# Kernel tuning notes

Hardware: AMD Instinct MI355X
Metric: run time of the kernel (lower is better)

## Reference

```python
import jax, jax.numpy as jnp
import numpy as np

E, T, IN, OUT, GS = 8, 2048, 2048, 2048, 64


def setup_inputs() -> dict:
    key = jax.random.key(0)
    k1, k2, k3, k4, k5 = jax.random.split(key, 5)
    x = jax.random.normal(k1, (T, IN), dtype=jnp.float32)
    # int4 codes in [0,16): stored unpacked as int32 for the reference
    qweight = jax.random.randint(k2, (E, IN, OUT), 0, 16, dtype=jnp.int32)
    G = IN // GS  # quant groups along the reduction dim
    scales = jax.random.uniform(k3, (E, G, OUT), jnp.float32, minval=0.005, maxval=0.02)
    zeros = jax.random.normal(k4, (E, G, OUT), jnp.float32) * 0.01
    scales_and_zeros = jnp.stack([scales, zeros], axis=-1)  # [E, G, OUT, 2]
    # tokens sorted by expert: per-expert counts are diffs of sorted cut points, sum == T
    cuts = jnp.sort(jax.random.randint(k5, (E - 1,), 0, T + 1, dtype=jnp.int32))
    bounds = jnp.concatenate([jnp.zeros((1,), jnp.int32), cuts, jnp.full((1,), T, jnp.int32)])
    tokens_per_expert = jnp.diff(bounds).astype(jnp.int32)  # [E]
    return {
        "x": x,
        "qweight": qweight,
        "scales_and_zeros": scales_and_zeros,
        "tokens_per_expert": tokens_per_expert,
        "group_size": GS,
    }


def reference(x, qweight, scales_and_zeros, tokens_per_expert, group_size):
    """Grouped (per-expert) int4 dequant + GEMM over an expert-sorted token matrix.

    Math of aten._weight_int4pack_mm per expert e over each quant group g:
        W_e[k, n] = (q_e[k, n] - 8) * scale_e[g, n] + zero_e[g, n],  g = k // group_size
        out[rows_e] = x[rows_e] @ W_e
    where rows_e is the contiguous slice given by cumsum(tokens_per_expert).
    """
    n_exp, in_f, out_f = qweight.shape
    n_tok = x.shape[0]
    G = in_f // group_size

    # dequantize all expert weights: [E, IN, OUT]
    q = qweight.reshape(n_exp, G, group_size, out_f).astype(x.dtype)
    scales = scales_and_zeros[..., 0][:, :, None, :]  # [E, G, 1, OUT]
    zeros = scales_and_zeros[..., 1][:, :, None, :]   # [E, G, 1, OUT]
    W = ((q - 8.0) * scales + zeros).reshape(n_exp, in_f, out_f)

    # expert id per token from the cumsum boundaries (tokens are expert-sorted)
    cum = jnp.cumsum(tokens_per_expert)                                # [E]
    eid = jnp.searchsorted(cum, jnp.arange(n_tok), side="right")       # [T]
    onehot = (eid[:, None] == jnp.arange(n_exp)[None, :]).astype(x.dtype)  # [T, E]

    # dispatch -> per-expert GEMM -> combine (jit-safe grouped GEMM)
    xe = jnp.einsum("te,ti->eti", onehot, x)       # [E, T, IN]
    ye = jnp.einsum("eti,eio->eto", xe, W)         # [E, T, OUT]
    out = jnp.einsum("te,eto->to", onehot, ye)     # [T, OUT]
    return out
```

## Files before the change

### kernel.cpp

```cpp
#include <hip/hip_runtime.h>
#include <hip/hip_bf16.h>

constexpr int NE  = 8;
constexpr int T   = 2048;
constexpr int IN  = 2048;
constexpr int OUT = 2048;
constexpr int GS  = 64;
constexpr int G   = IN / GS;

constexpr int BM = 128;
constexpr int BN = 64;
constexpr int BK = 64;
constexpr int NTILE = IN / BK;
constexpr int LDB = BK + 8;

using short8  = __attribute__((ext_vector_type(8))) short;
using short4v = __attribute__((ext_vector_type(4))) short;
using floatx4 = __attribute__((ext_vector_type(4))) float;
using int4v   = __attribute__((ext_vector_type(4))) int;
using float4v = __attribute__((ext_vector_type(4))) float;

__global__ __launch_bounds__(256)
void cvt_x_bf16(const float* __restrict__ x, __hip_bfloat16* __restrict__ xb) {
    const int i = (blockIdx.x * 256 + threadIdx.x) * 4;
    const float4 v = *(const float4*)(x + i);
    union { unsigned long long u; __hip_bfloat162 h2[2]; } p;
    p.h2[0] = __float22bfloat162_rn(float2{v.x, v.y});
    p.h2[1] = __float22bfloat162_rn(float2{v.z, v.w});
    *(unsigned long long*)(xb + i) = p.u;
}

__global__ __launch_bounds__(256, 4)
void hqq_grouped_gemm(const __hip_bfloat16* __restrict__ xb,
                      const int*   __restrict__ qw,
                      const float* __restrict__ snz,
                      const int*   __restrict__ tpe,
                      float* __restrict__ out) {
    const int tid = threadIdx.x;
    const int e   = blockIdx.z;
    const int tm  = blockIdx.y;
    const int n0  = blockIdx.x * BN;

    int b0 = 0;
#pragma unroll
    for (int i = 0; i < NE; ++i) { int c = tpe[i]; if (i < e) b0 += c; }
    const int b1 = b0 + tpe[e];
    const int row0 = b0 + tm * BM;
    if (row0 >= b1) return;

    __shared__ __hip_bfloat16 Bs[2][BN][LDB];

    floatx4 acc[2][4];
#pragma unroll
    for (int i = 0; i < 2; ++i)
#pragma unroll
        for (int j = 0; j < 4; ++j)
            acc[i][j] = (floatx4){0.f, 0.f, 0.f, 0.f};

    const int n4 = (tid & 15) * 4;
    const int kq = (tid >> 4) * 4;

    const int lane = tid & 63;
    const int wid  = tid >> 6;
    const int wm = wid * 32;
    const int lm = lane & 15;
    const int lk = (lane >> 4) * 8;

    const int*    qbase  = qw + (size_t)e * IN * OUT + n0 + n4;
    const float2* szbase = (const float2*)snz + (size_t)e * G * OUT + n0 + n4;

    int4v   qvA[4], qvB[4];
    float4v szA[2], szB[2];

    auto issue = [&](int t, int4v (&qv)[4], float4v (&sz)[2]) {
        const int k0 = t * BK;
        const float4v* szp = (const float4v*)(szbase + (size_t)(k0 >> 6) * OUT);
        sz[0] = szp[0];
        sz[1] = szp[1];
#pragma unroll
        for (int kk = 0; kk < 4; ++kk)
            qv[kk] = *(const int4v*)(qbase + (size_t)(k0 + kq + kk) * OUT);
    };

    auto stage = [&](__hip_bfloat16 (&B)[BN][LDB], int4v (&qv)[4], float4v (&sz)[2]) {
#pragma unroll
        for (int nn = 0; nn < 4; ++nn) {
            const float sc = sz[nn >> 1][(nn & 1) * 2];
            const float cc = sz[nn >> 1][(nn & 1) * 2 + 1] - 8.0f * sc;
            union { short4v v; __hip_bfloat162 h2[2]; } pb;
            pb.h2[0] = __float22bfloat162_rn(float2{(float)qv[0][nn] * sc + cc,
                                                    (float)qv[1][nn] * sc + cc});
            pb.h2[1] = __float22bfloat162_rn(float2{(float)qv[2][nn] * sc + cc,
                                                    (float)qv[3][nn] * sc + cc});
            *(short4v*)&B[n4 + nn][kq] = pb.v;
        }
    };

    auto mfma_tile = [&](const __hip_bfloat16 (&B)[BN][LDB], int k0) {
#pragma unroll
        for (int ks = 0; ks < BK; ks += 32) {
            short8 af[2], bfr[4];
#pragma unroll
            for (int i = 0; i < 2; ++i) {
                const int row = row0 + wm + i * 16 + lm;
                const int rr  = row < b1 ? row : (b1 - 1);
                af[i] = *(const short8*)(xb + (size_t)rr * IN + k0 + ks + lk);
            }
#pragma unroll
            for (int j = 0; j < 4; ++j)
                bfr[j] = *(const short8*)&B[j * 16 + lm][ks + lk];
#pragma unroll
            for (int i = 0; i < 2; ++i)
#pragma unroll
                for (int j = 0; j < 4; ++j)
                    acc[i][j] = __builtin_amdgcn_mfma_f32_16x16x32_bf16(
                        af[i], bfr[j], acc[i][j], 0, 0, 0);
        }
    };

#define TILE_SYNC()                                          \
    asm volatile("s_waitcnt lgkmcnt(0)" ::: "memory");       \
    __builtin_amdgcn_s_barrier();                            \
    __builtin_amdgcn_sched_barrier(0)

    issue(0, qvA, szA);

    for (int t = 0; t < NTILE; t += 2) {
        stage(Bs[0], qvA, szA);
        issue(t + 1, qvB, szB);
        TILE_SYNC();
        mfma_tile(Bs[0], t * BK);

        stage(Bs[1], qvB, szB);
        issue(t + 2 < NTILE ? t + 2 : t + 1, qvA, szA);
        TILE_SYNC();
        mfma_tile(Bs[1], (t + 1) * BK);
    }
#undef TILE_SYNC

    const int lq = (lane >> 4) * 4;
#pragma unroll
    for (int i = 0; i < 2; ++i) {
#pragma unroll
        for (int r = 0; r < 4; ++r) {
            const int row = row0 + wm + i * 16 + lq + r;
            if (row < b1) {
                float* op = out + (size_t)row * OUT + n0 + lm;
#pragma unroll
                for (int j = 0; j < 4; ++j)
                    op[j * 16] = acc[i][j][r];
            }
        }
    }
}

extern "C" void kernel_launch(void* const* d_in, const int* in_sizes, int n_in,
                              void* d_out, int out_size, void* d_ws, size_t ws_size,
                              hipStream_t stream) {
    const float* x   = (const float*)d_in[0];
    const int*   qw  = (const int*)d_in[1];
    const float* snz = (const float*)d_in[2];
    const int*   tpe = (const int*)d_in[3];
    float* out = (float*)d_out;
    __hip_bfloat16* xb = (__hip_bfloat16*)d_ws;

    cvt_x_bf16<<<(T * IN) / (256 * 4), 256, 0, stream>>>(x, xb);

    dim3 grid(OUT / BN, T / BM, NE);
    hqq_grouped_gemm<<<grid, 256, 0, stream>>>(xb, qw, snz, tpe, out);
}
```

Before: 265.2 us.

## Prefetch A fragments two tiles ahead and XOR-swizzle unpadded LDS B tile

Activation fragments for the MFMA now load into registers one to two tiles ahead instead of being fetched inside the compute loop. The quantized-weight prefetch is also deepened to two tiles in flight. The padded LDS row stride is replaced by an XOR swizzle on the k offset, which keeps bank-conflict avoidance while shrinking LDS. The extra live registers lead to lowering the launch-bounds occupancy hint from 4 to 3 blocks per CU.

```diff
diff --git a/kernel.cpp b/kernel.cpp
--- a/kernel.cpp
+++ b/kernel.cpp
@@ -12,7 +12,7 @@
 constexpr int BN = 64;
 constexpr int BK = 64;
 constexpr int NTILE = IN / BK;
-constexpr int LDB = BK + 8;
+constexpr int LDB = 64;
 
 using short8  = __attribute__((ext_vector_type(8))) short;
 using short4v = __attribute__((ext_vector_type(4))) short;
@@ -30,7 +30,7 @@
     *(unsigned long long*)(xb + i) = p.u;
 }
 
-__global__ __launch_bounds__(256, 4)
+__global__ __launch_bounds__(256, 3)
 void hqq_grouped_gemm(const __hip_bfloat16* __restrict__ xb,
                       const int*   __restrict__ qw,
                       const float* __restrict__ snz,
@@ -57,29 +57,45 @@
         for (int j = 0; j < 4; ++j)
             acc[i][j] = (floatx4){0.f, 0.f, 0.f, 0.f};
 
-    const int n4 = (tid & 15) * 4;
-    const int kq = (tid >> 4) * 4;
+    const int n4  = (tid & 15) * 4;
+    const int kq4 = (tid >> 4) * 4;
+    const int wsz = (tid & 3) << 4;
 
     const int lane = tid & 63;
     const int wid  = tid >> 6;
     const int wm = wid * 32;
     const int lm = lane & 15;
     const int lk = (lane >> 4) * 8;
+    const int rsz = ((lm >> 2) & 3) << 4;
 
     const int*    qbase  = qw + (size_t)e * IN * OUT + n0 + n4;
     const float2* szbase = (const float2*)snz + (size_t)e * G * OUT + n0 + n4;
 
+    const int r0c = min(row0 + wm + lm,      b1 - 1);
+    const int r1c = min(row0 + wm + 16 + lm, b1 - 1);
+    const __hip_bfloat16* ap0 = xb + (size_t)r0c * IN + lk;
+    const __hip_bfloat16* ap1 = xb + (size_t)r1c * IN + lk;
+
     int4v   qvA[4], qvB[4];
     float4v szA[2], szB[2];
+    short8  afA[4], afB[4];
 
-    auto issue = [&](int t, int4v (&qv)[4], float4v (&sz)[2]) {
+    auto issue_q = [&](int t, int4v (&qv)[4], float4v (&sz)[2]) {
         const int k0 = t * BK;
         const float4v* szp = (const float4v*)(szbase + (size_t)(k0 >> 6) * OUT);
         sz[0] = szp[0];
         sz[1] = szp[1];
 #pragma unroll
         for (int kk = 0; kk < 4; ++kk)
-            qv[kk] = *(const int4v*)(qbase + (size_t)(k0 + kq + kk) * OUT);
+            qv[kk] = *(const int4v*)(qbase + (size_t)(k0 + kq4 + kk) * OUT);
+    };
+
+    auto issue_af = [&](int t, short8 (&af)[4]) {
+        const int k0 = t * BK;
+        af[0] = *(const short8*)(ap0 + k0);
+        af[1] = *(const short8*)(ap1 + k0);
+        af[2] = *(const short8*)(ap0 + k0 + 32);
+        af[3] = *(const short8*)(ap1 + k0 + 32);
     };
 
     auto stage = [&](__hip_bfloat16 (&B)[BN][LDB], int4v (&qv)[4], float4v (&sz)[2]) {
@@ -92,29 +108,23 @@
                                                     (float)qv[1][nn] * sc + cc});
             pb.h2[1] = __float22bfloat162_rn(float2{(float)qv[2][nn] * sc + cc,
                                                     (float)qv[3][nn] * sc + cc});
-            *(short4v*)&B[n4 + nn][kq] = pb.v;
+            *(short4v*)&B[n4 + nn][kq4 ^ wsz] = pb.v;
         }
     };
 
-    auto mfma_tile = [&](const __hip_bfloat16 (&B)[BN][LDB], int k0) {
+    auto mfma_tile = [&](const __hip_bfloat16 (&B)[BN][LDB], const short8 (&af)[4]) {
 #pragma unroll
-        for (int ks = 0; ks < BK; ks += 32) {
-            short8 af[2], bfr[4];
-#pragma unroll
-            for (int i = 0; i < 2; ++i) {
-                const int row = row0 + wm + i * 16 + lm;
-                const int rr  = row < b1 ? row : (b1 - 1);
-                af[i] = *(const short8*)(xb + (size_t)rr * IN + k0 + ks + lk);
-            }
+        for (int ks2 = 0; ks2 < 2; ++ks2) {
+            short8 bfr[4];
 #pragma unroll
             for (int j = 0; j < 4; ++j)
-                bfr[j] = *(const short8*)&B[j * 16 + lm][ks + lk];
+                bfr[j] = *(const short8*)&B[j * 16 + lm][(ks2 * 32 + lk) ^ rsz];
 #pragma unroll
             for (int i = 0; i < 2; ++i)
 #pragma unroll
                 for (int j = 0; j < 4; ++j)
                     acc[i][j] = __builtin_amdgcn_mfma_f32_16x16x32_bf16(
-                        af[i], bfr[j], acc[i][j], 0, 0, 0);
+                        af[ks2 * 2 + i], bfr[j], acc[i][j], 0, 0, 0);
         }
     };
 
@@ -123,18 +133,23 @@
     __builtin_amdgcn_s_barrier();                            \
     __builtin_amdgcn_sched_barrier(0)
 
-    issue(0, qvA, szA);
+    issue_q(0, qvA, szA);
+    issue_q(1, qvB, szB);
+    issue_af(0, afA);
+    issue_af(1, afB);
 
     for (int t = 0; t < NTILE; t += 2) {
         stage(Bs[0], qvA, szA);
-        issue(t + 1, qvB, szB);
+        { const int tn = (t + 2 < NTILE) ? t + 2 : NTILE - 1; issue_q(tn, qvA, szA); }
         TILE_SYNC();
-        mfma_tile(Bs[0], t * BK);
+        mfma_tile(Bs[0], afA);
+        { const int tn = (t + 2 < NTILE) ? t + 2 : NTILE - 1; issue_af(tn, afA); }
 
         stage(Bs[1], qvB, szB);
-        issue(t + 2 < NTILE ? t + 2 : t + 1, qvA, szA);
+        { const int tn = (t + 3 < NTILE) ? t + 3 : NTILE - 1; issue_q(tn, qvB, szB); }
         TILE_SYNC();
-        mfma_tile(Bs[1], (t + 1) * BK);
+        mfma_tile(Bs[1], afB);
+        { const int tn = (t + 3 < NTILE) ? t + 3 : NTILE - 1; issue_af(tn, afB); }
     }
 #undef TILE_SYNC
 
```

New measurement: 254.6 us. 1.04x faster.
